# Optimization experiments

Hardware: AMD Instinct MI355X
Metric: run time of the kernel (lower is better)

Reference implementation:

```python
import jax, jax.numpy as jnp
import numpy as np

D_MODEL = 1024
N_HEADS = 16
D_K = 64
CHUNK_LEN = 64


def setup_inputs() -> dict:
    key = jax.random.key(0)
    ks = jax.random.split(key, 10)
    B, S = 4, 2048
    NC, NN, NL = 32, 2, 128
    s = 1.0 / np.sqrt(D_MODEL)
    inp = {
        "query": jax.random.normal(ks[0], (B, S, D_MODEL), dtype=jnp.float32),
        "key": jax.random.normal(ks[1], (B, NC, NN, NL, D_MODEL), dtype=jnp.float32),
        # Linear weights stored as [in, out] (equivalent to torch W.T)
        "Wq": jax.random.normal(ks[2], (D_MODEL, N_HEADS * D_K), dtype=jnp.float32) * s,
        "bq": jnp.zeros((N_HEADS * D_K,), dtype=jnp.float32),
        "Wk": jax.random.normal(ks[3], (D_MODEL, N_HEADS * D_K), dtype=jnp.float32) * s,
        "bk": jnp.zeros((N_HEADS * D_K,), dtype=jnp.float32),
        "Wv": jax.random.normal(ks[4], (D_MODEL, N_HEADS * D_K), dtype=jnp.float32) * s,
        "bv": jnp.zeros((N_HEADS * D_K,), dtype=jnp.float32),
        "Wo": jax.random.normal(ks[5], (N_HEADS * D_K, D_MODEL), dtype=jnp.float32) * s,
        "bo": jnp.zeros((D_MODEL,), dtype=jnp.float32),
    }
    return inp


def reference(query, key, Wq, bq, Wk, bk, Wv, bv, Wo, bo):
    B, S, D = query.shape
    _, NC, NN, NL, _ = key.shape
    L = NN * NL  # kv length per chunk
    # reshape query into chunks: [B, NC, chunk_len, D]
    q_in = query.reshape(B, NC, CHUNK_LEN, D)
    kv_in = key.reshape(B, NC, L, D)  # key used for both K and V in the original
    # projections, split heads: [B, NC, H, T, d_k]
    q = (q_in @ Wq + bq).reshape(B, NC, CHUNK_LEN, N_HEADS, D_K).transpose(0, 1, 3, 2, 4)
    k = (kv_in @ Wk + bk).reshape(B, NC, L, N_HEADS, D_K).transpose(0, 1, 3, 2, 4)
    v = (kv_in @ Wv + bv).reshape(B, NC, L, N_HEADS, D_K).transpose(0, 1, 3, 2, 4)
    # attention per (batch, chunk, head)
    scores = jnp.einsum("bchqd,bchkd->bchqk", q, k) / jnp.sqrt(jnp.float32(D_K))
    attn = jax.nn.softmax(scores, axis=-1)
    o = jnp.einsum("bchqk,bchkd->bchqd", attn, v)
    # merge heads: [B, NC, chunk_len, H*d_k]
    o = o.transpose(0, 1, 3, 2, 4).reshape(B, NC, CHUNK_LEN, N_HEADS * D_K)
    out = o @ Wo + bo
    return out.reshape(B, S, D)
```

## Files before the change

### kernel.cpp

```cpp
#include <hip/hip_runtime.h>
#include <hip/hip_bf16.h>
#include <stdint.h>

#define DMODEL 1024
#define NHEADS 16
#define DK 64
#define TQ 64
#define LKV 256
#define MQ 8192
#define MKV 32768

typedef __bf16 bf16x8 __attribute__((ext_vector_type(8)));
typedef float f32x4 __attribute__((ext_vector_type(4)));
typedef unsigned short u16x8 __attribute__((ext_vector_type(8)));
typedef unsigned short u16;

__device__ __forceinline__ unsigned short f2bf(float f) {
    union { float f; unsigned int i; } x; x.f = f;
    unsigned int r = (x.i + 0x7FFFu + ((x.i >> 16) & 1u)) >> 16;
    return (unsigned short)r;
}

__device__ __forceinline__ void gload_lds16(const void* g, void* l) {
    __builtin_amdgcn_global_load_lds(
        (const __attribute__((address_space(1))) unsigned int*)g,
        (__attribute__((address_space(3))) unsigned int*)l, 16, 0, 0);
}

__global__ __launch_bounds__(256) void cvt_f32_bf16(const float* __restrict__ in,
                                                    unsigned short* __restrict__ out) {
    long long i = ((long long)blockIdx.x * 256 + threadIdx.x) * 8;
    f32x4 a = *(const f32x4*)(in + i);
    f32x4 b = *(const f32x4*)(in + i + 4);
    u16x8 o;
    o[0] = f2bf(a[0]); o[1] = f2bf(a[1]); o[2] = f2bf(a[2]); o[3] = f2bf(a[3]);
    o[4] = f2bf(b[0]); o[5] = f2bf(b[1]); o[6] = f2bf(b[2]); o[7] = f2bf(b[3]);
    *(u16x8*)(out + i) = o;
}

__global__ __launch_bounds__(256) void transpose_w_cvt(const float* __restrict__ in,
                                                       unsigned short* __restrict__ out) {
    __shared__ float tile[64][65];
    int bi = blockIdx.y, bj = blockIdx.x;
    int tid = threadIdx.x;
    int c = tid & 63, r0 = tid >> 6;
#pragma unroll
    for (int p = 0; p < 16; ++p) {
        int r = r0 + 4 * p;
        tile[r][c] = in[(size_t)(bi * 64 + r) * 1024 + bj * 64 + c];
    }
    __syncthreads();
#pragma unroll
    for (int p = 0; p < 16; ++p) {
        int r = r0 + 4 * p;
        out[(size_t)(bj * 64 + r) * 1024 + bi * 64 + c] = f2bf(tile[c][r]);
    }
}

template <int OUTMODE>
__global__ __launch_bounds__(256) void gemm_bias(const unsigned short* __restrict__ A,
                                                 const unsigned short* __restrict__ Bt,
                                                 const float* __restrict__ bias,
                                                 void* __restrict__ OutV) {
    __shared__ alignas(16) unsigned short aLds[128 * 32];
    __shared__ alignas(16) unsigned short bLds[128 * 32];

    int tid = threadIdx.x;
    int lane = tid & 63, wid = tid >> 6;
    int m0 = blockIdx.x * 128;
    int n0 = blockIdx.y * 128;
    int wr = (wid >> 1) * 64, wc = (wid & 1) * 64;

    f32x4 zero = {0.f, 0.f, 0.f, 0.f};
    f32x4 acc[4][4];
#pragma unroll
    for (int i = 0; i < 4; ++i)
#pragma unroll
        for (int j = 0; j < 4; ++j) acc[i][j] = zero;

    int sr = lane >> 2;
    int sk = (lane & 3) * 8;
    const unsigned short* aG = A + (size_t)(m0 + sr) * 1024 + sk;
    const unsigned short* bG = Bt + (size_t)(n0 + sr) * 1024 + sk;
    int c0 = wid, c1 = wid + 4;

    int fr = lane & 15, fg = (lane >> 4) * 8;

    for (int kt = 0; kt < 1024; kt += 32) {
        gload_lds16(aG + (size_t)(c0 * 16) * 1024 + kt, aLds + c0 * 512);
        gload_lds16(aG + (size_t)(c1 * 16) * 1024 + kt, aLds + c1 * 512);
        gload_lds16(bG + (size_t)(c0 * 16) * 1024 + kt, bLds + c0 * 512);
        gload_lds16(bG + (size_t)(c1 * 16) * 1024 + kt, bLds + c1 * 512);
        __syncthreads();

        bf16x8 af[4], bf[4];
#pragma unroll
        for (int mt = 0; mt < 4; ++mt)
            af[mt] = *(const bf16x8*)&aLds[(wr + mt * 16 + fr) * 32 + fg];
#pragma unroll
        for (int nt = 0; nt < 4; ++nt)
            bf[nt] = *(const bf16x8*)&bLds[(wc + nt * 16 + fr) * 32 + fg];
#pragma unroll
        for (int mt = 0; mt < 4; ++mt)
#pragma unroll
            for (int nt = 0; nt < 4; ++nt)
                acc[mt][nt] = __builtin_amdgcn_mfma_f32_16x16x32_bf16(af[mt], bf[nt], acc[mt][nt], 0, 0, 0);
        __syncthreads();
    }

    float bv[4];
#pragma unroll
    for (int nt = 0; nt < 4; ++nt) bv[nt] = bias[n0 + wc + nt * 16 + fr];

    if (OUTMODE == 0) {
        unsigned short* Out = (unsigned short*)OutV;
#pragma unroll
        for (int mt = 0; mt < 4; ++mt)
#pragma unroll
            for (int r = 0; r < 4; ++r) {
                size_t row = (size_t)(m0 + wr + mt * 16 + (lane >> 4) * 4 + r);
#pragma unroll
                for (int nt = 0; nt < 4; ++nt)
                    Out[row * 1024 + n0 + wc + nt * 16 + fr] = f2bf(acc[mt][nt][r] + bv[nt]);
            }
    } else {
        float* Out = (float*)OutV;
#pragma unroll
        for (int mt = 0; mt < 4; ++mt)
#pragma unroll
            for (int r = 0; r < 4; ++r) {
                size_t row = (size_t)(m0 + wr + mt * 16 + (lane >> 4) * 4 + r);
#pragma unroll
                for (int nt = 0; nt < 4; ++nt)
                    Out[row * 1024 + n0 + wc + nt * 16 + fr] = acc[mt][nt][r] + bv[nt];
            }
    }
}


__device__ __forceinline__ void stageA64(const u16* src, u16* ldsTile, int row0, int tid) {
    int w = tid >> 6, l = tid & 63;
    int r = row0 + w * 8 + (l >> 3);
    int k16 = (l & 7) ^ ((l >> 3) & 7);
    gload_lds16(src + (size_t)r * 1024 + k16 * 8, ldsTile + (size_t)(row0 + w * 8) * 64);
}
__device__ __forceinline__ void stageB64(const u16* src, u16* ldsTile, int j, int odd, int tid) {
    int w = tid >> 6, l = tid & 63;
    int ib = j * 64 + w * 8;
    int rowbase = ((ib >> 5) << 6) + (ib & 31) + (odd ? 32 : 0);
    int r = rowbase + (l >> 3);
    int k16 = (l & 7) ^ ((l >> 3) & 7);
    gload_lds16(src + (size_t)r * 1024 + k16 * 8, ldsTile + (size_t)rowbase * 64);
}

#define VMWAIT2() asm volatile("s_waitcnt vmcnt(2)" ::: "memory")
#define SBAR()    do { __builtin_amdgcn_s_barrier(); asm volatile("" ::: "memory"); } while (0)

template <int OUTMODE>
__global__ __launch_bounds__(512, 2) void gemm256(const u16* __restrict__ A,
                                                  const u16* __restrict__ Bt,
                                                  const float* __restrict__ bias,
                                                  void* __restrict__ OutV, int nBx) {
    __shared__ alignas(16) u16 lds[65536];
    u16* ldsA0 = lds;          u16* ldsA1 = lds + 16384;
    u16* ldsB0 = lds + 32768;  u16* ldsB1 = lds + 49152;

    int tid = threadIdx.x, lane = tid & 63, wid = tid >> 6;
    int wm = wid >> 2, wn = wid & 3;

    int nB = nBx * 4;
    int bid = blockIdx.x;
    int qq = nB >> 3, rr = nB & 7;
    int xcd = bid & 7, idx = bid >> 3;
    int wg = (xcd < rr) ? xcd * (qq + 1) + idx : rr * (qq + 1) + (xcd - rr) * qq + idx;
    int m0 = (wg >> 2) * 256;
    int n0 = (wg & 3) * 256;

    const u16* aSrc = A + (size_t)m0 * 1024;
    const u16* bSrc = Bt + (size_t)n0 * 1024;

    f32x4 zero = {0.f, 0.f, 0.f, 0.f};
    f32x4 acc[8][4];
#pragma unroll
    for (int i = 0; i < 8; ++i)
#pragma unroll
        for (int j = 0; j < 4; ++j) acc[i][j] = zero;

    bf16x8 aR[4][2], b0R[2][2], b1R[2][2];

#define READ_A(lA, half)                                                         \
    do {                                                                         \
        _Pragma("unroll") for (int mf = 0; mf < 4; ++mf) {                       \
            int row = wm * 128 + (half) * 64 + mf * 16 + (lane & 15);            \
            _Pragma("unroll") for (int kk = 0; kk < 2; ++kk) {                   \
                int k16 = kk * 4 + (lane >> 4);                                  \
                aR[mf][kk] = *(const bf16x8*)&(lA)[row * 64 + ((k16 ^ (row & 7)) << 3)]; \
            }                                                                    \
        }                                                                        \
    } while (0)
#define READ_B(lB, half, dst)                                                    \
    do {                                                                         \
        _Pragma("unroll") for (int nf = 0; nf < 2; ++nf) {                       \
            int row = wn * 64 + (half) * 32 + nf * 16 + (lane & 15);             \
            _Pragma("unroll") for (int kk = 0; kk < 2; ++kk) {                   \
                int k16 = kk * 4 + (lane >> 4);                                  \
                dst[nf][kk] = *(const bf16x8*)&(lB)[row * 64 + ((k16 ^ (row & 7)) << 3)]; \
            }                                                                    \
        }                                                                        \
    } while (0)
#define MFMA16(mh, nh, bR)                                                       \
    do {                                                                         \
        __builtin_amdgcn_s_setprio(1);                                           \
        _Pragma("unroll") for (int mf = 0; mf < 4; ++mf)                         \
            _Pragma("unroll") for (int nf = 0; nf < 2; ++nf)                     \
                _Pragma("unroll") for (int kk = 0; kk < 2; ++kk)                 \
                    acc[(mh)*4 + mf][(nh)*2 + nf] =                              \
                        __builtin_amdgcn_mfma_f32_16x16x32_bf16(                 \
                            aR[mf][kk], bR[nf][kk], acc[(mh)*4 + mf][(nh)*2 + nf], 0, 0, 0); \
        __builtin_amdgcn_s_setprio(0);                                           \
    } while (0)

    stageA64(aSrc, ldsA0, 0, tid);    stageA64(aSrc, ldsA0, 128, tid);
    stageB64(bSrc, ldsB0, 0, 0, tid); stageB64(bSrc, ldsB0, 1, 0, tid);
    stageB64(bSrc, ldsB0, 0, 1, tid); stageB64(bSrc, ldsB0, 1, 1, tid);
    stageA64(aSrc, ldsA0, 64, tid);   stageA64(aSrc, ldsA0, 192, tid);
    asm volatile("s_waitcnt vmcnt(0)" ::: "memory");
    SBAR();

    for (int t = 0; t < 16; ++t) {
        int cur = t & 1;
        u16* lA = cur ? ldsA1 : ldsA0;
        u16* lB = cur ? ldsB1 : ldsB0;
        u16* pA = cur ? ldsA0 : ldsA1;
        u16* pB = cur ? ldsB0 : ldsB1;
        const u16* aNext = aSrc + (t + 1) * 64;
        const u16* bNext = bSrc + (t + 1) * 64;
        bool pf = (t < 15);

        VMWAIT2();
        READ_A(lA, 0);
        READ_B(lB, 0, b0R);
        if (pf) { stageA64(aNext, pA, 0, tid); stageA64(aNext, pA, 128, tid); }
        SBAR();
        MFMA16(0, 0, b0R);
        SBAR();

        VMWAIT2();
        READ_B(lB, 1, b1R);
        if (pf) { stageB64(bNext, pB, 0, 0, tid); stageB64(bNext, pB, 1, 0, tid); }
        SBAR();
        MFMA16(0, 1, b1R);
        SBAR();

        READ_A(lA, 1);
        if (pf) { stageB64(bNext, pB, 0, 1, tid); stageB64(bNext, pB, 1, 1, tid); }
        SBAR();
        MFMA16(1, 1, b1R);
        SBAR();

        VMWAIT2();
        if (pf) { stageA64(aNext, pA, 64, tid); stageA64(aNext, pA, 192, tid); }
        SBAR();
        MFMA16(1, 0, b0R);
        SBAR();
    }

    float bv[4];
#pragma unroll
    for (int NF = 0; NF < 4; ++NF) bv[NF] = bias[n0 + wn * 64 + NF * 16 + (lane & 15)];

    if (OUTMODE == 0) {
        u16* Out = (u16*)OutV;
#pragma unroll
        for (int MF = 0; MF < 8; ++MF)
#pragma unroll
            for (int r = 0; r < 4; ++r) {
                size_t row = (size_t)(m0 + wm * 128 + MF * 16 + (lane >> 4) * 4 + r);
#pragma unroll
                for (int NF = 0; NF < 4; ++NF)
                    Out[row * 1024 + n0 + wn * 64 + NF * 16 + (lane & 15)] =
                        f2bf(acc[MF][NF][r] + bv[NF]);
            }
    } else if (OUTMODE == 1) {
        u16* Out = (u16*)OutV;
#pragma unroll
        for (int MF = 0; MF < 8; ++MF)
#pragma unroll
            for (int r = 0; r < 4; ++r) {
                int gm = m0 + wm * 128 + MF * 16 + (lane >> 4) * 4 + r;
                int bc2 = gm >> 8, lv = gm & 255;
#pragma unroll
                for (int NF = 0; NF < 4; ++NF) {
                    int n = n0 + wn * 64 + NF * 16 + (lane & 15);
                    int hh = n >> 6, dd = n & 63;
                    Out[(size_t)((bc2 * 16 + hh) * 64 + dd) * 256 + lv] =
                        f2bf(acc[MF][NF][r] + bv[NF]);
                }
            }
    } else {
        float* Out = (float*)OutV;
#pragma unroll
        for (int MF = 0; MF < 8; ++MF)
#pragma unroll
            for (int r = 0; r < 4; ++r) {
                size_t row = (size_t)(m0 + wm * 128 + MF * 16 + (lane >> 4) * 4 + r);
#pragma unroll
                for (int NF = 0; NF < 4; ++NF)
                    Out[row * 1024 + n0 + wn * 64 + NF * 16 + (lane & 15)] =
                        acc[MF][NF][r] + bv[NF];
            }
    }
#undef READ_A
#undef READ_B
#undef MFMA16
}

__global__ __launch_bounds__(256) void attn_kernel(const unsigned short* __restrict__ Q,
                                                   const unsigned short* __restrict__ K,
                                                   const unsigned short* __restrict__ Vt,
                                                   unsigned short* O) {
    __shared__ alignas(16) unsigned short pLds[64 * 264];

    int tid = threadIdx.x;
    int lane = tid & 63, w = tid >> 6;
    int bc = blockIdx.x >> 4, h = blockIdx.x & 15;
    int fr = lane & 15, g = lane >> 4;

    const unsigned short* qb = Q + (size_t)(bc * 64 + w * 16 + fr) * 1024 + h * 64 + g * 8;
    bf16x8 qf0 = *(const bf16x8*)qb;
    bf16x8 qf1 = *(const bf16x8*)(qb + 32);

    const unsigned short* kb = K + (size_t)(bc * 256 + fr) * 1024 + h * 64 + g * 8;

    f32x4 zero = {0.f, 0.f, 0.f, 0.f};
    f32x4 sc[16];
#pragma unroll
    for (int nt = 0; nt < 16; ++nt) sc[nt] = zero;

#pragma unroll
    for (int nt = 0; nt < 16; ++nt) {
        bf16x8 kf0 = *(const bf16x8*)(kb + (size_t)(nt * 16) * 1024);
        bf16x8 kf1 = *(const bf16x8*)(kb + (size_t)(nt * 16) * 1024 + 32);
        sc[nt] = __builtin_amdgcn_mfma_f32_16x16x32_bf16(qf0, kf0, sc[nt], 0, 0, 0);
        sc[nt] = __builtin_amdgcn_mfma_f32_16x16x32_bf16(qf1, kf1, sc[nt], 0, 0, 0);
    }

    const float scale = 0.125f;
    float mx[4], sum[4];
#pragma unroll
    for (int r = 0; r < 4; ++r) {
        float m = -1e30f;
#pragma unroll
        for (int nt = 0; nt < 16; ++nt) {
            sc[nt][r] *= scale;
            m = fmaxf(m, sc[nt][r]);
        }
#pragma unroll
        for (int x = 1; x < 16; x <<= 1) m = fmaxf(m, __shfl_xor(m, x, 64));
        mx[r] = m;
        sum[r] = 0.f;
    }
#pragma unroll
    for (int nt = 0; nt < 16; ++nt)
#pragma unroll
        for (int r = 0; r < 4; ++r) {
            float p = __expf(sc[nt][r] - mx[r]);
            sum[r] += p;
            pLds[(w * 16 + g * 4 + r) * 264 + nt * 16 + fr] = f2bf(p);
        }
#pragma unroll
    for (int r = 0; r < 4; ++r)
#pragma unroll
        for (int x = 1; x < 16; x <<= 1) sum[r] += __shfl_xor(sum[r], x, 64);

    __syncthreads();

    f32x4 oa[4];
#pragma unroll
    for (int nt = 0; nt < 4; ++nt) oa[nt] = zero;

    const unsigned short* vtb = Vt + (size_t)((bc * 16 + h) * 64) * 256;
#pragma unroll
    for (int ks = 0; ks < 8; ++ks) {
        bf16x8 pf = *(const bf16x8*)&pLds[(w * 16 + fr) * 264 + ks * 32 + g * 8];
#pragma unroll
        for (int nt = 0; nt < 4; ++nt) {
            bf16x8 vf = *(const bf16x8*)(vtb + (size_t)(nt * 16 + fr) * 256 + ks * 32 + g * 8);
            oa[nt] = __builtin_amdgcn_mfma_f32_16x16x32_bf16(pf, vf, oa[nt], 0, 0, 0);
        }
    }

    float rs[4];
#pragma unroll
    for (int r = 0; r < 4; ++r) rs[r] = 1.0f / sum[r];

    unsigned short* ob = O + (size_t)(bc * 64 + w * 16 + g * 4) * 1024 + h * 64 + fr;
#pragma unroll
    for (int nt = 0; nt < 4; ++nt)
#pragma unroll
        for (int r = 0; r < 4; ++r)
            ob[(size_t)r * 1024 + nt * 16] = f2bf(oa[nt][r] * rs[r]);
}

extern "C" void kernel_launch(void* const* d_in, const int* in_sizes, int n_in,
                              void* d_out, int out_size, void* d_ws, size_t ws_size,
                              hipStream_t stream) {
    const float* query = (const float*)d_in[0];
    const float* keyin = (const float*)d_in[1];
    const float* Wq = (const float*)d_in[2];
    const float* bq = (const float*)d_in[3];
    const float* Wk = (const float*)d_in[4];
    const float* bk = (const float*)d_in[5];
    const float* Wv = (const float*)d_in[6];
    const float* bv = (const float*)d_in[7];
    const float* Wo = (const float*)d_in[8];
    const float* bo = (const float*)d_in[9];

    unsigned short* ws = (unsigned short*)d_ws;
    const size_t MB1 = 1024 * 1024;

    unsigned short* WqT = ws;
    unsigned short* WkT = ws + MB1;
    unsigned short* WvT = ws + 2 * MB1;
    unsigned short* WoT = ws + 3 * MB1;
    unsigned short* qb16 = ws + 4 * MB1;
    unsigned short* Qp   = qb16 + (size_t)MQ * 1024;
    unsigned short* kvb  = Qp + (size_t)MQ * 1024;

    size_t ws_elems = ws_size / 2;
    size_t fixed = 4 * MB1 + 2 * (size_t)MQ * 1024;
    size_t avail = (ws_elems > fixed) ? (ws_elems - fixed) : 0;
    long long max_rows = (long long)(avail / (3 * 1024));
    int slice_rows = (int)((max_rows / 256) * 256);
    if (slice_rows > MKV) slice_rows = MKV;
    if (slice_rows < 256) slice_rows = 256;

    unsigned short* Kp = kvb + (size_t)slice_rows * 1024;
    unsigned short* Vt = Kp + (size_t)slice_rows * 1024;

    dim3 tb(256);
    transpose_w_cvt<<<dim3(16, 16), tb, 0, stream>>>(Wq, WqT);
    transpose_w_cvt<<<dim3(16, 16), tb, 0, stream>>>(Wk, WkT);
    transpose_w_cvt<<<dim3(16, 16), tb, 0, stream>>>(Wv, WvT);
    transpose_w_cvt<<<dim3(16, 16), tb, 0, stream>>>(Wo, WoT);

    cvt_f32_bf16<<<dim3(MQ * 1024 / (256 * 8)), tb, 0, stream>>>(query, qb16);
    gemm_bias<0><<<dim3(MQ / 128, 8), tb, 0, stream>>>(qb16, WqT, bq, Qp);

    for (int r0 = 0; r0 < MKV; r0 += slice_rows) {
        int rows = MKV - r0;
        if (rows > slice_rows) rows = slice_rows;
        cvt_f32_bf16<<<dim3(rows * 1024 / (256 * 8)), tb, 0, stream>>>(
            keyin + (size_t)r0 * 1024, kvb);
        gemm256<0><<<dim3((rows / 256) * 4), dim3(512), 0, stream>>>(kvb, WkT, bk, Kp, rows / 256);
        gemm256<1><<<dim3((rows / 256) * 4), dim3(512), 0, stream>>>(kvb, WvT, bv, Vt, rows / 256);
        size_t qoff = (size_t)(r0 / 4) * 1024;
        attn_kernel<<<dim3((rows / 256) * 16), tb, 0, stream>>>(
            Qp + qoff, Kp, Vt, Qp + qoff);
    }

    gemm_bias<2><<<dim3(MQ / 128, 8), tb, 0, stream>>>(Qp, WoT, bo, d_out);
}
```

Before: 328.6 us.

## Fuse fp32-to-bf16 conversion into GEMM A-operand loads and merge weight transposes

The gemm256 kernel now reads fp32 activations directly, converts them to bf16 in registers and writes them to LDS. This removes the separate cvt_f32_bf16 passes over query and key and their bf16 staging buffers. The pipeline is rebuilt as register-prefetched A plus LDS-staged B with one barrier per K-step, and the Q projection now uses gemm256 instead of the smaller gemm_bias. The four weight transposes are merged into one launch. In exchange, the key is read in fp32 twice (once for K, once for V), doubling that activation traffic, and register pressure goes up.

```diff
diff --git a/kernel.cpp b/kernel.cpp
--- a/kernel.cpp
+++ b/kernel.cpp
@@ -12,7 +12,6 @@
 
 typedef __bf16 bf16x8 __attribute__((ext_vector_type(8)));
 typedef float f32x4 __attribute__((ext_vector_type(4)));
-typedef unsigned short u16x8 __attribute__((ext_vector_type(8)));
 typedef unsigned short u16;
 
 __device__ __forceinline__ unsigned short f2bf(float f) {
@@ -27,20 +26,22 @@
         (__attribute__((address_space(3))) unsigned int*)l, 16, 0, 0);
 }
 
-__global__ __launch_bounds__(256) void cvt_f32_bf16(const float* __restrict__ in,
-                                                    unsigned short* __restrict__ out) {
-    long long i = ((long long)blockIdx.x * 256 + threadIdx.x) * 8;
-    f32x4 a = *(const f32x4*)(in + i);
-    f32x4 b = *(const f32x4*)(in + i + 4);
-    u16x8 o;
-    o[0] = f2bf(a[0]); o[1] = f2bf(a[1]); o[2] = f2bf(a[2]); o[3] = f2bf(a[3]);
-    o[4] = f2bf(b[0]); o[5] = f2bf(b[1]); o[6] = f2bf(b[2]); o[7] = f2bf(b[3]);
-    *(u16x8*)(out + i) = o;
-}
-
-__global__ __launch_bounds__(256) void transpose_w_cvt(const float* __restrict__ in,
-                                                       unsigned short* __restrict__ out) {
+__global__ __launch_bounds__(256) void transpose_w_cvt4(const float* __restrict__ w0,
+                                                        const float* __restrict__ w1,
+                                                        const float* __restrict__ w2,
+                                                        const float* __restrict__ w3,
+                                                        u16* __restrict__ o0,
+                                                        u16* __restrict__ o1,
+                                                        u16* __restrict__ o2,
+                                                        u16* __restrict__ o3) {
     __shared__ float tile[64][65];
+    const float* in; u16* out;
+    switch (blockIdx.z) {
+        case 0: in = w0; out = o0; break;
+        case 1: in = w1; out = o1; break;
+        case 2: in = w2; out = o2; break;
+        default: in = w3; out = o3; break;
+    }
     int bi = blockIdx.y, bj = blockIdx.x;
     int tid = threadIdx.x;
     int c = tid & 63, r0 = tid >> 6;
@@ -58,12 +59,12 @@
 }
 
 template <int OUTMODE>
-__global__ __launch_bounds__(256) void gemm_bias(const unsigned short* __restrict__ A,
-                                                 const unsigned short* __restrict__ Bt,
+__global__ __launch_bounds__(256) void gemm_bias(const u16* __restrict__ A,
+                                                 const u16* __restrict__ Bt,
                                                  const float* __restrict__ bias,
                                                  void* __restrict__ OutV) {
-    __shared__ alignas(16) unsigned short aLds[128 * 32];
-    __shared__ alignas(16) unsigned short bLds[128 * 32];
+    __shared__ alignas(16) u16 aLds[128 * 32];
+    __shared__ alignas(16) u16 bLds[128 * 32];
 
     int tid = threadIdx.x;
     int lane = tid & 63, wid = tid >> 6;
@@ -80,8 +81,8 @@
 
     int sr = lane >> 2;
     int sk = (lane & 3) * 8;
-    const unsigned short* aG = A + (size_t)(m0 + sr) * 1024 + sk;
-    const unsigned short* bG = Bt + (size_t)(n0 + sr) * 1024 + sk;
+    const u16* aG = A + (size_t)(m0 + sr) * 1024 + sk;
+    const u16* bG = Bt + (size_t)(n0 + sr) * 1024 + sk;
     int c0 = wid, c1 = wid + 4;
 
     int fr = lane & 15, fg = (lane >> 4) * 8;
@@ -113,7 +114,7 @@
     for (int nt = 0; nt < 4; ++nt) bv[nt] = bias[n0 + wc + nt * 16 + fr];
 
     if (OUTMODE == 0) {
-        unsigned short* Out = (unsigned short*)OutV;
+        u16* Out = (u16*)OutV;
 #pragma unroll
         for (int mt = 0; mt < 4; ++mt)
 #pragma unroll
@@ -138,12 +139,6 @@
 }
 
 
-__device__ __forceinline__ void stageA64(const u16* src, u16* ldsTile, int row0, int tid) {
-    int w = tid >> 6, l = tid & 63;
-    int r = row0 + w * 8 + (l >> 3);
-    int k16 = (l & 7) ^ ((l >> 3) & 7);
-    gload_lds16(src + (size_t)r * 1024 + k16 * 8, ldsTile + (size_t)(row0 + w * 8) * 64);
-}
 __device__ __forceinline__ void stageB64(const u16* src, u16* ldsTile, int j, int odd, int tid) {
     int w = tid >> 6, l = tid & 63;
     int ib = j * 64 + w * 8;
@@ -153,11 +148,8 @@
     gload_lds16(src + (size_t)r * 1024 + k16 * 8, ldsTile + (size_t)rowbase * 64);
 }
 
-#define VMWAIT2() asm volatile("s_waitcnt vmcnt(2)" ::: "memory")
-#define SBAR()    do { __builtin_amdgcn_s_barrier(); asm volatile("" ::: "memory"); } while (0)
-
 template <int OUTMODE>
-__global__ __launch_bounds__(512, 2) void gemm256(const u16* __restrict__ A,
+__global__ __launch_bounds__(512, 2) void gemm256(const float* __restrict__ A,
                                                   const u16* __restrict__ Bt,
                                                   const float* __restrict__ bias,
                                                   void* __restrict__ OutV, int nBx) {
@@ -176,8 +168,12 @@
     int m0 = (wg >> 2) * 256;
     int n0 = (wg & 3) * 256;
 
-    const u16* aSrc = A + (size_t)m0 * 1024;
+    const float* aSrc = A + (size_t)m0 * 1024;
     const u16* bSrc = Bt + (size_t)n0 * 1024;
+
+    int l3 = lane >> 3;
+    size_t aRowOff = (size_t)(wid * 8 + l3) * 1024 + (lane & 7) * 8;
+    int aLdsOff = (wid * 8 + l3) * 64 + (((lane & 7) ^ (l3 & 7)) << 3);
 
     f32x4 zero = {0.f, 0.f, 0.f, 0.f};
     f32x4 acc[8][4];
@@ -186,83 +182,126 @@
 #pragma unroll
         for (int j = 0; j < 4; ++j) acc[i][j] = zero;
 
-    bf16x8 aR[4][2], b0R[2][2], b1R[2][2];
-
-#define READ_A(lA, half)                                                         \
+    f32x4 rA[8], rB[8];
+    bf16x8 aR4[4], b0[2], b1[2];
+
+#define A_ISSUE(R, T)                                                            \
+    do {                                                                         \
+        const float* _p = aSrc + (size_t)(T) * 64 + aRowOff;                     \
+        _Pragma("unroll") for (int c = 0; c < 4; ++c) {                          \
+            R[2 * c]     = *(const f32x4*)(_p + (size_t)c * 64 * 1024);          \
+            R[2 * c + 1] = *(const f32x4*)(_p + (size_t)c * 64 * 1024 + 4);      \
+        }                                                                        \
+    } while (0)
+#define A_WRITE(R, L)                                                            \
+    do {                                                                         \
+        _Pragma("unroll") for (int c = 0; c < 4; ++c) {                          \
+            bf16x8 _v;                                                           \
+            _Pragma("unroll") for (int j = 0; j < 4; ++j) {                      \
+                _v[j]     = (__bf16)R[2 * c][j];                                 \
+                _v[4 + j] = (__bf16)R[2 * c + 1][j];                             \
+            }                                                                    \
+            *(bf16x8*)&(L)[aLdsOff + c * 64 * 64] = _v;                          \
+        }                                                                        \
+    } while (0)
+#define B_STAGE(L, T)                                                            \
+    do {                                                                         \
+        const u16* _b = bSrc + (size_t)(T) * 64;                                 \
+        stageB64(_b, (L), 0, 0, tid); stageB64(_b, (L), 1, 0, tid);              \
+        stageB64(_b, (L), 0, 1, tid); stageB64(_b, (L), 1, 1, tid);              \
+    } while (0)
+#define READ_A4(L, HALF, KK)                                                     \
     do {                                                                         \
         _Pragma("unroll") for (int mf = 0; mf < 4; ++mf) {                       \
-            int row = wm * 128 + (half) * 64 + mf * 16 + (lane & 15);            \
-            _Pragma("unroll") for (int kk = 0; kk < 2; ++kk) {                   \
-                int k16 = kk * 4 + (lane >> 4);                                  \
-                aR[mf][kk] = *(const bf16x8*)&(lA)[row * 64 + ((k16 ^ (row & 7)) << 3)]; \
-            }                                                                    \
+            int row = wm * 128 + (HALF) * 64 + mf * 16 + (lane & 15);            \
+            int k16 = (KK) * 4 + (lane >> 4);                                    \
+            aR4[mf] = *(const bf16x8*)&(L)[row * 64 + ((k16 ^ (row & 7)) << 3)]; \
         }                                                                        \
     } while (0)
-#define READ_B(lB, half, dst)                                                    \
+#define READ_B2(BB, L, NH, KK)                                                   \
     do {                                                                         \
         _Pragma("unroll") for (int nf = 0; nf < 2; ++nf) {                       \
-            int row = wn * 64 + (half) * 32 + nf * 16 + (lane & 15);             \
-            _Pragma("unroll") for (int kk = 0; kk < 2; ++kk) {                   \
-                int k16 = kk * 4 + (lane >> 4);                                  \
-                dst[nf][kk] = *(const bf16x8*)&(lB)[row * 64 + ((k16 ^ (row & 7)) << 3)]; \
-            }                                                                    \
+            int row = wn * 64 + (NH) * 32 + nf * 16 + (lane & 15);               \
+            int k16 = (KK) * 4 + (lane >> 4);                                    \
+            BB[nf] = *(const bf16x8*)&(L)[row * 64 + ((k16 ^ (row & 7)) << 3)];  \
         }                                                                        \
     } while (0)
-#define MFMA16(mh, nh, bR)                                                       \
+#define MFMA8(MH, NH, BB)                                                        \
     do {                                                                         \
         __builtin_amdgcn_s_setprio(1);                                           \
         _Pragma("unroll") for (int mf = 0; mf < 4; ++mf)                         \
             _Pragma("unroll") for (int nf = 0; nf < 2; ++nf)                     \
-                _Pragma("unroll") for (int kk = 0; kk < 2; ++kk)                 \
-                    acc[(mh)*4 + mf][(nh)*2 + nf] =                              \
-                        __builtin_amdgcn_mfma_f32_16x16x32_bf16(                 \
-                            aR[mf][kk], bR[nf][kk], acc[(mh)*4 + mf][(nh)*2 + nf], 0, 0, 0); \
+                acc[(MH) * 4 + mf][(NH) * 2 + nf] =                              \
+                    __builtin_amdgcn_mfma_f32_16x16x32_bf16(                     \
+                        aR4[mf], BB[nf], acc[(MH) * 4 + mf][(NH) * 2 + nf], 0, 0, 0); \
         __builtin_amdgcn_s_setprio(0);                                           \
     } while (0)
-
-    stageA64(aSrc, ldsA0, 0, tid);    stageA64(aSrc, ldsA0, 128, tid);
-    stageB64(bSrc, ldsB0, 0, 0, tid); stageB64(bSrc, ldsB0, 1, 0, tid);
-    stageB64(bSrc, ldsB0, 0, 1, tid); stageB64(bSrc, ldsB0, 1, 1, tid);
-    stageA64(aSrc, ldsA0, 64, tid);   stageA64(aSrc, ldsA0, 192, tid);
-    asm volatile("s_waitcnt vmcnt(0)" ::: "memory");
-    SBAR();
-
-    for (int t = 0; t < 16; ++t) {
-        int cur = t & 1;
-        u16* lA = cur ? ldsA1 : ldsA0;
-        u16* lB = cur ? ldsB1 : ldsB0;
-        u16* pA = cur ? ldsA0 : ldsA1;
-        u16* pB = cur ? ldsB0 : ldsB1;
-        const u16* aNext = aSrc + (t + 1) * 64;
-        const u16* bNext = bSrc + (t + 1) * 64;
-        bool pf = (t < 15);
-
-        VMWAIT2();
-        READ_A(lA, 0);
-        READ_B(lB, 0, b0R);
-        if (pf) { stageA64(aNext, pA, 0, tid); stageA64(aNext, pA, 128, tid); }
-        SBAR();
-        MFMA16(0, 0, b0R);
-        SBAR();
-
-        VMWAIT2();
-        READ_B(lB, 1, b1R);
-        if (pf) { stageB64(bNext, pB, 0, 0, tid); stageB64(bNext, pB, 1, 0, tid); }
-        SBAR();
-        MFMA16(0, 1, b1R);
-        SBAR();
-
-        READ_A(lA, 1);
-        if (pf) { stageB64(bNext, pB, 0, 1, tid); stageB64(bNext, pB, 1, 1, tid); }
-        SBAR();
-        MFMA16(1, 1, b1R);
-        SBAR();
-
-        VMWAIT2();
-        if (pf) { stageA64(aNext, pA, 64, tid); stageA64(aNext, pA, 192, tid); }
-        SBAR();
-        MFMA16(1, 0, b0R);
-        SBAR();
+#define COMPUTE(L)                                                               \
+    do {                                                                         \
+        _Pragma("unroll") for (int kk = 0; kk < 2; ++kk) {                       \
+            READ_A4(L, 0, kk);                                                   \
+            READ_B2(b0, L, 0, kk);                                               \
+            READ_B2(b1, L, 1, kk);                                               \
+            MFMA8(0, 0, b0);                                                     \
+            MFMA8(0, 1, b1);                                                     \
+            READ_A4(L, 1, kk);                                                   \
+            MFMA8(1, 1, b1);                                                     \
+            MFMA8(1, 0, b0);                                                     \
+        }                                                                        \
+    } while (0)
+#define FENCE() asm volatile("" ::: "memory")
+#define BODY(T, LCA, LCB, LNA, LNB, RW, RI)                                      \
+    do {                                                                         \
+        A_WRITE(RW, LNA);                                                        \
+        B_STAGE(LNB, (T) + 1);                                                   \
+        FENCE();                                                                 \
+        if ((T) < 14) A_ISSUE(RI, (T) + 2);                                      \
+        FENCE();                                                                 \
+        COMPUTE(LCA);                                                            \
+        if ((T) < 14) { asm volatile("s_waitcnt vmcnt(8) lgkmcnt(0)" ::: "memory"); } \
+        else          { asm volatile("s_waitcnt vmcnt(0) lgkmcnt(0)" ::: "memory"); } \
+        __builtin_amdgcn_s_barrier();                                            \
+        FENCE();                                                                 \
+    } while (0)
+
+    A_ISSUE(rA, 0);
+    A_WRITE(rA, ldsA0);
+    B_STAGE(ldsB0, 0);
+    FENCE();
+    A_ISSUE(rB, 1);
+    FENCE();
+    asm volatile("s_waitcnt vmcnt(8) lgkmcnt(0)" ::: "memory");
+    __builtin_amdgcn_s_barrier();
+    FENCE();
+
+#define BODY_EVEN(T) do { A_WRITE(rB, ldsA1); B_STAGE(ldsB1, (T) + 1); FENCE();  \
+        if ((T) < 14) A_ISSUE(rA, (T) + 2); FENCE();                             \
+        _Pragma("unroll") for (int kk = 0; kk < 2; ++kk) {                       \
+            READ_A4(ldsA0, 0, kk); READ_B2(b0, ldsB0, 0, kk); READ_B2(b1, ldsB0, 1, kk); \
+            MFMA8(0, 0, b0); MFMA8(0, 1, b1);                                    \
+            READ_A4(ldsA0, 1, kk); MFMA8(1, 1, b1); MFMA8(1, 0, b0); }           \
+        if ((T) < 14) { asm volatile("s_waitcnt vmcnt(8) lgkmcnt(0)" ::: "memory"); } \
+        else          { asm volatile("s_waitcnt vmcnt(0) lgkmcnt(0)" ::: "memory"); } \
+        __builtin_amdgcn_s_barrier(); FENCE(); } while (0)
+#define BODY_ODD(T) do { A_WRITE(rA, ldsA0); B_STAGE(ldsB0, (T) + 1); FENCE();   \
+        A_ISSUE(rB, (T) + 2); FENCE();                                           \
+        _Pragma("unroll") for (int kk = 0; kk < 2; ++kk) {                       \
+            READ_A4(ldsA1, 0, kk); READ_B2(b0, ldsB1, 0, kk); READ_B2(b1, ldsB1, 1, kk); \
+            MFMA8(0, 0, b0); MFMA8(0, 1, b1);                                    \
+            READ_A4(ldsA1, 1, kk); MFMA8(1, 1, b1); MFMA8(1, 0, b0); }           \
+        asm volatile("s_waitcnt vmcnt(8) lgkmcnt(0)" ::: "memory");              \
+        __builtin_amdgcn_s_barrier(); FENCE(); } while (0)
+
+    for (int t = 0; t < 14; t += 2) {
+        BODY_EVEN(t);
+        BODY_ODD(t + 1);
+    }
+    BODY_EVEN(14);
+#pragma unroll
+    for (int kk = 0; kk < 2; ++kk) {
+        READ_A4(ldsA1, 0, kk); READ_B2(b0, ldsB1, 0, kk); READ_B2(b1, ldsB1, 1, kk);
+        MFMA8(0, 0, b0); MFMA8(0, 1, b1);
+        READ_A4(ldsA1, 1, kk); MFMA8(1, 1, b1); MFMA8(1, 0, b0);
     }
 
     float bv[4];
@@ -281,7 +320,7 @@
                     Out[row * 1024 + n0 + wn * 64 + NF * 16 + (lane & 15)] =
                         f2bf(acc[MF][NF][r] + bv[NF]);
             }
-    } else if (OUTMODE == 1) {
+    } else {
         u16* Out = (u16*)OutV;
 #pragma unroll
         for (int MF = 0; MF < 8; ++MF)
@@ -297,40 +336,36 @@
                         f2bf(acc[MF][NF][r] + bv[NF]);
                 }
             }
-    } else {
-        float* Out = (float*)OutV;
-#pragma unroll
-        for (int MF = 0; MF < 8; ++MF)
-#pragma unroll
-            for (int r = 0; r < 4; ++r) {
-                size_t row = (size_t)(m0 + wm * 128 + MF * 16 + (lane >> 4) * 4 + r);
-#pragma unroll
-                for (int NF = 0; NF < 4; ++NF)
-                    Out[row * 1024 + n0 + wn * 64 + NF * 16 + (lane & 15)] =
-                        acc[MF][NF][r] + bv[NF];
-            }
-    }
-#undef READ_A
-#undef READ_B
-#undef MFMA16
-}
-
-__global__ __launch_bounds__(256) void attn_kernel(const unsigned short* __restrict__ Q,
-                                                   const unsigned short* __restrict__ K,
-                                                   const unsigned short* __restrict__ Vt,
-                                                   unsigned short* O) {
-    __shared__ alignas(16) unsigned short pLds[64 * 264];
+    }
+#undef A_ISSUE
+#undef A_WRITE
+#undef B_STAGE
+#undef READ_A4
+#undef READ_B2
+#undef MFMA8
+#undef COMPUTE
+#undef FENCE
+#undef BODY
+#undef BODY_EVEN
+#undef BODY_ODD
+}
+
+__global__ __launch_bounds__(256) void attn_kernel(const u16* __restrict__ Q,
+                                                   const u16* __restrict__ K,
+                                                   const u16* __restrict__ Vt,
+                                                   u16* O) {
+    __shared__ alignas(16) u16 pLds[64 * 264];
 
     int tid = threadIdx.x;
     int lane = tid & 63, w = tid >> 6;
     int bc = blockIdx.x >> 4, h = blockIdx.x & 15;
     int fr = lane & 15, g = lane >> 4;
 
-    const unsigned short* qb = Q + (size_t)(bc * 64 + w * 16 + fr) * 1024 + h * 64 + g * 8;
+    const u16* qb = Q + (size_t)(bc * 64 + w * 16 + fr) * 1024 + h * 64 + g * 8;
     bf16x8 qf0 = *(const bf16x8*)qb;
     bf16x8 qf1 = *(const bf16x8*)(qb + 32);
 
-    const unsigned short* kb = K + (size_t)(bc * 256 + fr) * 1024 + h * 64 + g * 8;
+    const u16* kb = K + (size_t)(bc * 256 + fr) * 1024 + h * 64 + g * 8;
 
     f32x4 zero = {0.f, 0.f, 0.f, 0.f};
     f32x4 sc[16];
@@ -379,7 +414,7 @@
 #pragma unroll
     for (int nt = 0; nt < 4; ++nt) oa[nt] = zero;
 
-    const unsigned short* vtb = Vt + (size_t)((bc * 16 + h) * 64) * 256;
+    const u16* vtb = Vt + (size_t)((bc * 16 + h) * 64) * 256;
 #pragma unroll
     for (int ks = 0; ks < 8; ++ks) {
         bf16x8 pf = *(const bf16x8*)&pLds[(w * 16 + fr) * 264 + ks * 32 + g * 8];
@@ -394,7 +429,7 @@
 #pragma unroll
     for (int r = 0; r < 4; ++r) rs[r] = 1.0f / sum[r];
 
-    unsigned short* ob = O + (size_t)(bc * 64 + w * 16 + g * 4) * 1024 + h * 64 + fr;
+    u16* ob = O + (size_t)(bc * 64 + w * 16 + g * 4) * 1024 + h * 64 + fr;
 #pragma unroll
     for (int nt = 0; nt < 4; ++nt)
 #pragma unroll
@@ -416,44 +451,37 @@
     const float* Wo = (const float*)d_in[8];
     const float* bo = (const float*)d_in[9];
 
-    unsigned short* ws = (unsigned short*)d_ws;
+    u16* ws = (u16*)d_ws;
     const size_t MB1 = 1024 * 1024;
 
-    unsigned short* WqT = ws;
-    unsigned short* WkT = ws + MB1;
-    unsigned short* WvT = ws + 2 * MB1;
-    unsigned short* WoT = ws + 3 * MB1;
-    unsigned short* qb16 = ws + 4 * MB1;
-    unsigned short* Qp   = qb16 + (size_t)MQ * 1024;
-    unsigned short* kvb  = Qp + (size_t)MQ * 1024;
+    u16* WqT = ws;
+    u16* WkT = ws + MB1;
+    u16* WvT = ws + 2 * MB1;
+    u16* WoT = ws + 3 * MB1;
+    u16* Qp  = ws + 4 * MB1;
+    u16* Kp  = Qp + (size_t)MQ * 1024;
 
     size_t ws_elems = ws_size / 2;
-    size_t fixed = 4 * MB1 + 2 * (size_t)MQ * 1024;
+    size_t fixed = 4 * MB1 + (size_t)MQ * 1024;
     size_t avail = (ws_elems > fixed) ? (ws_elems - fixed) : 0;
-    long long max_rows = (long long)(avail / (3 * 1024));
+    long long max_rows = (long long)(avail / (2 * 1024));
     int slice_rows = (int)((max_rows / 256) * 256);
     if (slice_rows > MKV) slice_rows = MKV;
     if (slice_rows < 256) slice_rows = 256;
 
-    unsigned short* Kp = kvb + (size_t)slice_rows * 1024;
-    unsigned short* Vt = Kp + (size_t)slice_rows * 1024;
+    u16* Vt = Kp + (size_t)slice_rows * 1024;
 
     dim3 tb(256);
-    transpose_w_cvt<<<dim3(16, 16), tb, 0, stream>>>(Wq, WqT);
-    transpose_w_cvt<<<dim3(16, 16), tb, 0, stream>>>(Wk, WkT);
-    transpose_w_cvt<<<dim3(16, 16), tb, 0, stream>>>(Wv, WvT);
-    transpose_w_cvt<<<dim3(16, 16), tb, 0, stream>>>(Wo, WoT);
-
-    cvt_f32_bf16<<<dim3(MQ * 1024 / (256 * 8)), tb, 0, stream>>>(query, qb16);
-    gemm_bias<0><<<dim3(MQ / 128, 8), tb, 0, stream>>>(qb16, WqT, bq, Qp);
+    transpose_w_cvt4<<<dim3(16, 16, 4), tb, 0, stream>>>(Wq, Wk, Wv, Wo, WqT, WkT, WvT, WoT);
+
+    gemm256<0><<<dim3((MQ / 256) * 4), dim3(512), 0, stream>>>(query, WqT, bq, Qp, MQ / 256);
 
     for (int r0 = 0; r0 < MKV; r0 += slice_rows) {
         int rows = MKV - r0;
         if (rows > slice_rows) rows = slice_rows;
-        cvt_f32_bf16<<<dim3(rows * 1024 / (256 * 8)), tb, 0, stream>>>(
-            keyin + (size_t)r0 * 1024, kvb);
-        gemm256<0><<<dim3((rows / 256) * 4), dim3(512), 0, stream>>>(kvb, WkT, bk, Kp, rows / 256);
-        gemm256<1><<<dim3((rows / 256) * 4), dim3(512), 0, stream>>>(kvb, WvT, bv, Vt, rows / 256);
+        const float* kvA = keyin + (size_t)r0 * 1024;
+        gemm256<0><<<dim3((rows / 256) * 4), dim3(512), 0, stream>>>(kvA, WkT, bk, Kp, rows / 256);
+        gemm256<1><<<dim3((rows / 256) * 4), dim3(512), 0, stream>>>(kvA, WvT, bv, Vt, rows / 256);
         size_t qoff = (size_t)(r0 / 4) * 1024;
         attn_kernel<<<dim3((rows / 256) * 16), tb, 0, stream>>>(
             Qp + qoff, Kp, Vt, Qp + qoff);
```

Result: no change. 332.1 us (+1.1%).

## Fuse Q, K, V projections into one launch and batch weight transposes

Applied to the files above, without the earlier changes.

Merges the K and V projection GEMMs with the Q projection into a single grouped launch, with each workgroup picking its operand set by index. Q now uses the 256-tile pipelined kernel instead of the smaller 128-tile GEMM, and the four weight transpose launches become one 3D-grid launch. Slice size is capped at 16384 rows when the workspace cannot hold all of KV. This cuts launch count and tail underfill but adds per-block branching and a runtime mode flag in the epilogue.

```diff
diff --git a/kernel.cpp b/kernel.cpp
--- a/kernel.cpp
+++ b/kernel.cpp
@@ -38,9 +38,22 @@
     *(u16x8*)(out + i) = o;
 }
 
-__global__ __launch_bounds__(256) void transpose_w_cvt(const float* __restrict__ in,
-                                                       unsigned short* __restrict__ out) {
+__global__ __launch_bounds__(256) void transpose_w_cvt4(const float* __restrict__ w0,
+                                                        const float* __restrict__ w1,
+                                                        const float* __restrict__ w2,
+                                                        const float* __restrict__ w3,
+                                                        u16* __restrict__ o0,
+                                                        u16* __restrict__ o1,
+                                                        u16* __restrict__ o2,
+                                                        u16* __restrict__ o3) {
     __shared__ float tile[64][65];
+    const float* in; u16* out;
+    switch (blockIdx.z) {
+        case 0: in = w0; out = o0; break;
+        case 1: in = w1; out = o1; break;
+        case 2: in = w2; out = o2; break;
+        default: in = w3; out = o3; break;
+    }
     int bi = blockIdx.y, bj = blockIdx.x;
     int tid = threadIdx.x;
     int c = tid & 63, r0 = tid >> 6;
@@ -58,12 +71,12 @@
 }
 
 template <int OUTMODE>
-__global__ __launch_bounds__(256) void gemm_bias(const unsigned short* __restrict__ A,
-                                                 const unsigned short* __restrict__ Bt,
+__global__ __launch_bounds__(256) void gemm_bias(const u16* __restrict__ A,
+                                                 const u16* __restrict__ Bt,
                                                  const float* __restrict__ bias,
                                                  void* __restrict__ OutV) {
-    __shared__ alignas(16) unsigned short aLds[128 * 32];
-    __shared__ alignas(16) unsigned short bLds[128 * 32];
+    __shared__ alignas(16) u16 aLds[128 * 32];
+    __shared__ alignas(16) u16 bLds[128 * 32];
 
     int tid = threadIdx.x;
     int lane = tid & 63, wid = tid >> 6;
@@ -80,8 +93,8 @@
 
     int sr = lane >> 2;
     int sk = (lane & 3) * 8;
-    const unsigned short* aG = A + (size_t)(m0 + sr) * 1024 + sk;
-    const unsigned short* bG = Bt + (size_t)(n0 + sr) * 1024 + sk;
+    const u16* aG = A + (size_t)(m0 + sr) * 1024 + sk;
+    const u16* bG = Bt + (size_t)(n0 + sr) * 1024 + sk;
     int c0 = wid, c1 = wid + 4;
 
     int fr = lane & 15, fg = (lane >> 4) * 8;
@@ -113,7 +126,7 @@
     for (int nt = 0; nt < 4; ++nt) bv[nt] = bias[n0 + wc + nt * 16 + fr];
 
     if (OUTMODE == 0) {
-        unsigned short* Out = (unsigned short*)OutV;
+        u16* Out = (u16*)OutV;
 #pragma unroll
         for (int mt = 0; mt < 4; ++mt)
 #pragma unroll
@@ -154,13 +167,21 @@
 }
 
 #define VMWAIT2() asm volatile("s_waitcnt vmcnt(2)" ::: "memory")
+#define VMWAIT0() asm volatile("s_waitcnt vmcnt(0)" ::: "memory")
 #define SBAR()    do { __builtin_amdgcn_s_barrier(); asm volatile("" ::: "memory"); } while (0)
 
-template <int OUTMODE>
-__global__ __launch_bounds__(512, 2) void gemm256(const u16* __restrict__ A,
-                                                  const u16* __restrict__ Bt,
-                                                  const float* __restrict__ bias,
-                                                  void* __restrict__ OutV, int nBx) {
+__global__ __launch_bounds__(512, 2) void proj_fused(const u16* __restrict__ Akv,
+                                                     const u16* __restrict__ Aq,
+                                                     const u16* __restrict__ WkT,
+                                                     const u16* __restrict__ WvT,
+                                                     const u16* __restrict__ WqT,
+                                                     const float* __restrict__ bk,
+                                                     const float* __restrict__ bv,
+                                                     const float* __restrict__ bq,
+                                                     u16* __restrict__ Kp,
+                                                     u16* __restrict__ Vt,
+                                                     u16* __restrict__ Qp,
+                                                     int nmKV, int nmQ) {
     __shared__ alignas(16) u16 lds[65536];
     u16* ldsA0 = lds;          u16* ldsA1 = lds + 16384;
     u16* ldsB0 = lds + 32768;  u16* ldsB1 = lds + 49152;
@@ -168,16 +189,23 @@
     int tid = threadIdx.x, lane = tid & 63, wid = tid >> 6;
     int wm = wid >> 2, wn = wid & 3;
 
-    int nB = nBx * 4;
+    int nB = gridDim.x;
     int bid = blockIdx.x;
     int qq = nB >> 3, rr = nB & 7;
     int xcd = bid & 7, idx = bid >> 3;
     int wg = (xcd < rr) ? xcd * (qq + 1) + idx : rr * (qq + 1) + (xcd - rr) * qq + idx;
-    int m0 = (wg >> 2) * 256;
-    int n0 = (wg & 3) * 256;
+
+    const u16* A; const u16* B; const float* bias; u16* Out; int mode;
+    int nKV4 = nmKV * 4;
+    int lwg;
+    if (wg < nKV4)            { lwg = wg;            A = Akv; B = WkT; bias = bk; Out = Kp; mode = 0; }
+    else if (wg < 2 * nKV4)   { lwg = wg - nKV4;     A = Akv; B = WvT; bias = bv; Out = Vt; mode = 1; }
+    else                      { lwg = wg - 2 * nKV4; A = Aq;  B = WqT; bias = bq; Out = Qp; mode = 0; }
+    int m0 = (lwg >> 2) * 256;
+    int n0 = (lwg & 3) * 256;
 
     const u16* aSrc = A + (size_t)m0 * 1024;
-    const u16* bSrc = Bt + (size_t)n0 * 1024;
+    const u16* bSrc = B + (size_t)n0 * 1024;
 
     f32x4 zero = {0.f, 0.f, 0.f, 0.f};
     f32x4 acc[8][4];
@@ -224,7 +252,7 @@
     stageB64(bSrc, ldsB0, 0, 0, tid); stageB64(bSrc, ldsB0, 1, 0, tid);
     stageB64(bSrc, ldsB0, 0, 1, tid); stageB64(bSrc, ldsB0, 1, 1, tid);
     stageA64(aSrc, ldsA0, 64, tid);   stageA64(aSrc, ldsA0, 192, tid);
-    asm volatile("s_waitcnt vmcnt(0)" ::: "memory");
+    VMWAIT0();
     SBAR();
 
     for (int t = 0; t < 16; ++t) {
@@ -245,7 +273,7 @@
         MFMA16(0, 0, b0R);
         SBAR();
 
-        VMWAIT2();
+        if (pf) { VMWAIT2(); } else { VMWAIT0(); }
         READ_B(lB, 1, b1R);
         if (pf) { stageB64(bNext, pB, 0, 0, tid); stageB64(bNext, pB, 1, 0, tid); }
         SBAR();
@@ -258,19 +286,20 @@
         MFMA16(1, 1, b1R);
         SBAR();
 
-        VMWAIT2();
-        if (pf) { stageA64(aNext, pA, 64, tid); stageA64(aNext, pA, 192, tid); }
+        if (pf) {
+            VMWAIT2();
+            stageA64(aNext, pA, 64, tid); stageA64(aNext, pA, 192, tid);
+        }
         SBAR();
         MFMA16(1, 0, b0R);
         SBAR();
     }
 
-    float bv[4];
-#pragma unroll
-    for (int NF = 0; NF < 4; ++NF) bv[NF] = bias[n0 + wn * 64 + NF * 16 + (lane & 15)];
-
-    if (OUTMODE == 0) {
-        u16* Out = (u16*)OutV;
+    float bvv[4];
+#pragma unroll
+    for (int NF = 0; NF < 4; ++NF) bvv[NF] = bias[n0 + wn * 64 + NF * 16 + (lane & 15)];
+
+    if (mode == 0) {
 #pragma unroll
         for (int MF = 0; MF < 8; ++MF)
 #pragma unroll
@@ -279,10 +308,9 @@
 #pragma unroll
                 for (int NF = 0; NF < 4; ++NF)
                     Out[row * 1024 + n0 + wn * 64 + NF * 16 + (lane & 15)] =
-                        f2bf(acc[MF][NF][r] + bv[NF]);
+                        f2bf(acc[MF][NF][r] + bvv[NF]);
             }
-    } else if (OUTMODE == 1) {
-        u16* Out = (u16*)OutV;
+    } else {
 #pragma unroll
         for (int MF = 0; MF < 8; ++MF)
 #pragma unroll
@@ -294,20 +322,8 @@
                     int n = n0 + wn * 64 + NF * 16 + (lane & 15);
                     int hh = n >> 6, dd = n & 63;
                     Out[(size_t)((bc2 * 16 + hh) * 64 + dd) * 256 + lv] =
-                        f2bf(acc[MF][NF][r] + bv[NF]);
+                        f2bf(acc[MF][NF][r] + bvv[NF]);
                 }
-            }
-    } else {
-        float* Out = (float*)OutV;
-#pragma unroll
-        for (int MF = 0; MF < 8; ++MF)
-#pragma unroll
-            for (int r = 0; r < 4; ++r) {
-                size_t row = (size_t)(m0 + wm * 128 + MF * 16 + (lane >> 4) * 4 + r);
-#pragma unroll
-                for (int NF = 0; NF < 4; ++NF)
-                    Out[row * 1024 + n0 + wn * 64 + NF * 16 + (lane & 15)] =
-                        acc[MF][NF][r] + bv[NF];
             }
     }
 #undef READ_A
@@ -315,22 +331,22 @@
 #undef MFMA16
 }
 
-__global__ __launch_bounds__(256) void attn_kernel(const unsigned short* __restrict__ Q,
-                                                   const unsigned short* __restrict__ K,
-                                                   const unsigned short* __restrict__ Vt,
-                                                   unsigned short* O) {
-    __shared__ alignas(16) unsigned short pLds[64 * 264];
+__global__ __launch_bounds__(256) void attn_kernel(const u16* __restrict__ Q,
+                                                   const u16* __restrict__ K,
+                                                   const u16* __restrict__ Vt,
+                                                   u16* O) {
+    __shared__ alignas(16) u16 pLds[64 * 264];
 
     int tid = threadIdx.x;
     int lane = tid & 63, w = tid >> 6;
     int bc = blockIdx.x >> 4, h = blockIdx.x & 15;
     int fr = lane & 15, g = lane >> 4;
 
-    const unsigned short* qb = Q + (size_t)(bc * 64 + w * 16 + fr) * 1024 + h * 64 + g * 8;
+    const u16* qb = Q + (size_t)(bc * 64 + w * 16 + fr) * 1024 + h * 64 + g * 8;
     bf16x8 qf0 = *(const bf16x8*)qb;
     bf16x8 qf1 = *(const bf16x8*)(qb + 32);
 
-    const unsigned short* kb = K + (size_t)(bc * 256 + fr) * 1024 + h * 64 + g * 8;
+    const u16* kb = K + (size_t)(bc * 256 + fr) * 1024 + h * 64 + g * 8;
 
     f32x4 zero = {0.f, 0.f, 0.f, 0.f};
     f32x4 sc[16];
@@ -379,7 +395,7 @@
 #pragma unroll
     for (int nt = 0; nt < 4; ++nt) oa[nt] = zero;
 
-    const unsigned short* vtb = Vt + (size_t)((bc * 16 + h) * 64) * 256;
+    const u16* vtb = Vt + (size_t)((bc * 16 + h) * 64) * 256;
 #pragma unroll
     for (int ks = 0; ks < 8; ++ks) {
         bf16x8 pf = *(const bf16x8*)&pLds[(w * 16 + fr) * 264 + ks * 32 + g * 8];
@@ -394,7 +410,7 @@
 #pragma unroll
     for (int r = 0; r < 4; ++r) rs[r] = 1.0f / sum[r];
 
-    unsigned short* ob = O + (size_t)(bc * 64 + w * 16 + g * 4) * 1024 + h * 64 + fr;
+    u16* ob = O + (size_t)(bc * 64 + w * 16 + g * 4) * 1024 + h * 64 + fr;
 #pragma unroll
     for (int nt = 0; nt < 4; ++nt)
 #pragma unroll
@@ -416,44 +432,42 @@
     const float* Wo = (const float*)d_in[8];
     const float* bo = (const float*)d_in[9];
 
-    unsigned short* ws = (unsigned short*)d_ws;
+    u16* ws = (u16*)d_ws;
     const size_t MB1 = 1024 * 1024;
 
-    unsigned short* WqT = ws;
-    unsigned short* WkT = ws + MB1;
-    unsigned short* WvT = ws + 2 * MB1;
-    unsigned short* WoT = ws + 3 * MB1;
-    unsigned short* qb16 = ws + 4 * MB1;
-    unsigned short* Qp   = qb16 + (size_t)MQ * 1024;
-    unsigned short* kvb  = Qp + (size_t)MQ * 1024;
+    u16* WqT = ws;
+    u16* WkT = ws + MB1;
+    u16* WvT = ws + 2 * MB1;
+    u16* WoT = ws + 3 * MB1;
+    u16* qb16 = ws + 4 * MB1;
+    u16* Qp   = qb16 + (size_t)MQ * 1024;
+    u16* kvb  = Qp + (size_t)MQ * 1024;
 
     size_t ws_elems = ws_size / 2;
     size_t fixed = 4 * MB1 + 2 * (size_t)MQ * 1024;
     size_t avail = (ws_elems > fixed) ? (ws_elems - fixed) : 0;
     long long max_rows = (long long)(avail / (3 * 1024));
     int slice_rows = (int)((max_rows / 256) * 256);
-    if (slice_rows > MKV) slice_rows = MKV;
+    if (slice_rows >= MKV) slice_rows = MKV;
+    else if (slice_rows >= 16384) slice_rows = 16384;
     if (slice_rows < 256) slice_rows = 256;
 
-    unsigned short* Kp = kvb + (size_t)slice_rows * 1024;
-    unsigned short* Vt = Kp + (size_t)slice_rows * 1024;
+    u16* Kp = kvb + (size_t)slice_rows * 1024;
+    u16* Vt = Kp + (size_t)slice_rows * 1024;
 
     dim3 tb(256);
-    transpose_w_cvt<<<dim3(16, 16), tb, 0, stream>>>(Wq, WqT);
-    transpose_w_cvt<<<dim3(16, 16), tb, 0, stream>>>(Wk, WkT);
-    transpose_w_cvt<<<dim3(16, 16), tb, 0, stream>>>(Wv, WvT);
-    transpose_w_cvt<<<dim3(16, 16), tb, 0, stream>>>(Wo, WoT);
-
+    transpose_w_cvt4<<<dim3(16, 16, 4), tb, 0, stream>>>(Wq, Wk, Wv, Wo, WqT, WkT, WvT, WoT);
     cvt_f32_bf16<<<dim3(MQ * 1024 / (256 * 8)), tb, 0, stream>>>(query, qb16);
-    gemm_bias<0><<<dim3(MQ / 128, 8), tb, 0, stream>>>(qb16, WqT, bq, Qp);
 
     for (int r0 = 0; r0 < MKV; r0 += slice_rows) {
         int rows = MKV - r0;
         if (rows > slice_rows) rows = slice_rows;
         cvt_f32_bf16<<<dim3(rows * 1024 / (256 * 8)), tb, 0, stream>>>(
             keyin + (size_t)r0 * 1024, kvb);
-        gemm256<0><<<dim3((rows / 256) * 4), dim3(512), 0, stream>>>(kvb, WkT, bk, Kp, rows / 256);
-        gemm256<1><<<dim3((rows / 256) * 4), dim3(512), 0, stream>>>(kvb, WvT, bv, Vt, rows / 256);
+        int nmKV = rows / 256;
+        int nmQ = (r0 == 0) ? (MQ / 256) : 0;
+        proj_fused<<<dim3(nmKV * 8 + nmQ * 4), dim3(512), 0, stream>>>(
+            kvb, qb16, WkT, WvT, WqT, bk, bv, bq, Kp, Vt, Qp, nmKV, nmQ);
         size_t qoff = (size_t)(r0 / 4) * 1024;
         attn_kernel<<<dim3((rows / 256) * 16), tb, 0, stream>>>(
             Qp + qoff, Kp, Vt, Qp + qoff);
```

Result: faster. 322.0 us (-2.0%).
